# Optimization experiments

Hardware: AMD Instinct MI355X
Metric: run time of the kernel (lower is better)

The kernel has to match this reference:

```python
import jax, jax.numpy as jnp
import numpy as np

N = 50000      # nodes
T = 4          # snapshots
F_IN = 128     # in_channels
H_DIM = 128    # hidden_channels
E = 800000     # edges per snapshot
K = 3          # Chebyshev order


def _edge_norm(src, dst, n):
    # PyG ChebConv sym normalization with lambda_max=2.0:
    # L_hat = L - I = -D^{-1/2} A D^{-1/2}  (diagonal of L_hat is 0)
    ones = jnp.ones(src.shape[0], jnp.float32)
    deg = jax.ops.segment_sum(ones, src, num_segments=n)
    dinv = jnp.where(deg > 0, jax.lax.rsqrt(deg), 0.0)
    return -dinv[src] * dinv[dst]


def _cheb_conv(x, src, dst, w, W, b):
    # x:(N,Fi), W:(K,Fi,Fo), b:(Fo,). Tx_0=x, Tx_1=L_hat x, Tx_k=2 L_hat Tx_{k-1} - Tx_{k-2}
    n = x.shape[0]

    def prop(t):  # sparse matmul L_hat @ t via gather-scale-scatter
        return jax.ops.segment_sum(w[:, None] * t[src], dst, num_segments=n)

    Tx0 = x
    out = Tx0 @ W[0]
    Tx1 = prop(Tx0)
    out = out + Tx1 @ W[1]
    for k in range(2, K):
        Tx2 = 2.0 * prop(Tx1) - Tx0
        out = out + Tx2 @ W[k]
        Tx0, Tx1 = Tx1, Tx2
    return out + b


def setup_inputs() -> dict:
    key = jax.random.key(0)
    ks = jax.random.split(key, 12)
    x = jax.random.normal(ks[0], (T, N, F_IN), jnp.float32)
    edge_index = jax.random.randint(ks[1], (T, 2, E), 0, N, dtype=jnp.int64)

    def w(k, fi, fo):
        return jax.random.normal(k, (K, fi, fo), jnp.float32) * 0.05

    inp = {
        "x": x, "edge_index": edge_index,
        "Wxz": w(ks[2], F_IN, H_DIM), "Whz": w(ks[3], H_DIM, H_DIM),
        "Wxr": w(ks[4], F_IN, H_DIM), "Whr": w(ks[5], H_DIM, H_DIM),
        "Wxh": w(ks[6], F_IN, H_DIM), "Whh": w(ks[7], H_DIM, H_DIM),
        "bxz": jnp.zeros(H_DIM, jnp.float32), "bhz": jnp.zeros(H_DIM, jnp.float32),
        "bxr": jnp.zeros(H_DIM, jnp.float32), "bhr": jnp.zeros(H_DIM, jnp.float32),
        "bxh": jnp.zeros(H_DIM, jnp.float32), "bhh": jnp.zeros(H_DIM, jnp.float32),
        "Wd1": jax.random.normal(ks[8], (H_DIM, H_DIM), jnp.float32) * 0.05,
        "bd1": jnp.zeros(H_DIM, jnp.float32),
        "Wd2": jax.random.normal(ks[9], (H_DIM, F_IN), jnp.float32) * 0.05,
        "bd2": jnp.zeros(F_IN, jnp.float32),
    }
    return inp


def reference(x, edge_index, Wxz, Whz, Wxr, Whr, Wxh, Whh,
              bxz, bhz, bxr, bhr, bxh, bhh, Wd1, bd1, Wd2, bd2):
    n = x.shape[1]

    def step(H, inp):
        xt, ei = inp
        src, dst = ei[0], ei[1]
        w = _edge_norm(src, dst, n)
        Z = jax.nn.sigmoid(_cheb_conv(xt, src, dst, w, Wxz, bxz)
                           + _cheb_conv(H, src, dst, w, Whz, bhz))
        R = jax.nn.sigmoid(_cheb_conv(xt, src, dst, w, Wxr, bxr)
                           + _cheb_conv(H, src, dst, w, Whr, bhr))
        Ht = jnp.tanh(_cheb_conv(xt, src, dst, w, Wxh, bxh)
                      + _cheb_conv(H * R, src, dst, w, Whh, bhh))
        H = Z * H + (1.0 - Z) * Ht
        return H, None

    H0 = jnp.zeros((n, H_DIM), x.dtype)
    H, _ = jax.lax.scan(step, H0, (x, edge_index))
    # decoder (dropout is identity at inference)
    x_pred = jax.nn.relu(H @ Wd1 + bd1) @ Wd2 + bd2
    return x_pred, H
```

## Files before the change

kernel.cpp:

```cpp
#include <hip/hip_runtime.h>
#include <math.h>

#define NN 50000
#define TT 4
#define FF 128
#define EE 800000
#define NSEG 4
#define BINSEG 12500
#define NCH 32
#define CHUNK 25000
#define NCH2 128
#define CH2 6250
#define NB2 64
#define CB 782
#define NSEG2 16
#define SEGW 3125
#define SBINS (CB*NSEG2)
#define SCHUNK 49
#define SMAX 13312
#define SPB 2048

typedef __attribute__((ext_vector_type(8))) short bf8_t;
typedef __attribute__((ext_vector_type(4))) float f4_t;
typedef __attribute__((ext_vector_type(8))) ushort us8;

__device__ inline ushort f2bf(float f){
  union { float f; unsigned u; } v; v.f = f;
  unsigned u = v.u;
  unsigned r = (u + 0x7fff + ((u>>16)&1)) >> 16;
  return (ushort)r;
}
__device__ inline float lo16(unsigned u){ union{unsigned u;float f;}v; v.u=u<<16; return v.f; }
__device__ inline float hi16(unsigned u){ union{unsigned u;float f;}v; v.u=u&0xffff0000u; return v.f; }
__device__ inline unsigned packbf(float x, float y){
  return (unsigned)f2bf(x) | ((unsigned)f2bf(y)<<16);
}
__device__ inline float sigm(float x){ return 1.f/(1.f+expf(-x)); }


__global__ void k_cast4(const float* __restrict__ in, ushort* __restrict__ outp, int n4){
  int i = blockIdx.x*256 + threadIdx.x;
  if(i<n4){
    float4 v = ((const float4*)in)[i];
    ushort4 o; o.x=f2bf(v.x); o.y=f2bf(v.y); o.z=f2bf(v.z); o.w=f2bf(v.w);
    int t = i / (NN*32);
    int rem = i - t*(NN*32);
    int r = rem >> 5;
    int f = (rem & 31) * 4;
    *(ushort4*)(outp + (size_t)t*NN*128 + ((size_t)(f>>5)*NN + r)*32 + (f&31)) = o;
  }
}
__global__ void k_bias(const float* bxz, const float* bhz, const float* bxr,
                       const float* bhr, const float* bxh, const float* bhh,
                       float* __restrict__ bz, float* __restrict__ br, float* __restrict__ bh){
  int i = threadIdx.x;
  int c = i & 127, s = i >> 7;
  if(s==0) bz[c]=bxz[c]+bhz[c];
  else if(s==1) br[c]=bxr[c]+bhr[c];
  else bh[c]=bxh[c]+bhh[c];
}

__global__ __launch_bounds__(256) void k_hist(const int* __restrict__ ei,
                                              int* __restrict__ part){
  int c = blockIdx.x, seg = blockIdx.y, t = blockIdx.z;
  const int* keys = ei + (size_t)t*2*EE;
  __shared__ int h[BINSEG];
  for(int i=threadIdx.x;i<BINSEG;i+=256) h[i]=0;
  __syncthreads();
  int base = seg*BINSEG;
  int e0 = c*CHUNK, e1 = e0+CHUNK;
  for(int e=e0+threadIdx.x; e<e1; e+=256){
    int k = keys[e] - base;
    if((unsigned)k < (unsigned)BINSEG) atomicAdd(&h[k],1);
  }
  __syncthreads();
  int* dp = part + ((((size_t)t)*NSEG + seg)*NCH + c)*BINSEG;
  for(int i=threadIdx.x;i<BINSEG;i+=256) dp[i]=h[i];
}
__global__ void k_merge(const int* __restrict__ part, float* __restrict__ dinv4){
  int t = blockIdx.y;
  int n = blockIdx.x*256 + threadIdx.x;
  if(n>=NN) return;
  int seg = n / BINSEG, b = n - seg*BINSEG;
  const int* p = part + ((((size_t)t)*NSEG + seg)*NCH)*BINSEG + b;
  int s = 0;
  #pragma unroll
  for(int c=0;c<NCH;++c) s += p[(size_t)c*BINSEG];
  dinv4[(size_t)t*NN + n] = s>0 ? rsqrtf((float)s) : 0.f;
}

__global__ __launch_bounds__(256) void k_ccount(const int* __restrict__ ei,
                                                int* __restrict__ ccnt){
  int c = blockIdx.x, t = blockIdx.y;
  const int* dst = ei + (size_t)t*2*EE + EE;
  __shared__ int h[NB2];
  if(threadIdx.x<NB2) h[threadIdx.x]=0;
  __syncthreads();
  int e0 = c*CH2, e1 = e0+CH2;
  for(int e=e0+threadIdx.x; e<e1; e+=256) atomicAdd(&h[dst[e]/CB],1);
  __syncthreads();
  if(threadIdx.x<NB2) ccnt[((size_t)t*NB2 + threadIdx.x)*NCH2 + c] = h[threadIdx.x];
}
__global__ __launch_bounds__(128) void k_cscan(const int* __restrict__ ccnt,
                        int* __restrict__ Abase, int* __restrict__ Bbase,
                        int* __restrict__ tot){
  int t = blockIdx.x, tid = threadIdx.x;
  __shared__ int st[NB2];
  __shared__ int sb[NB2];
  const int* cc = ccnt + (size_t)t*NB2*NCH2;
  if(tid<NB2){
    int s=0;
    for(int c=0;c<NCH2;++c) s += cc[tid*NCH2+c];
    st[tid]=s;
  }
  __syncthreads();
  if(tid==0){
    int run=0;
    for(int b=0;b<NB2;++b){ sb[b]=run; run+=st[b]; }
  }
  __syncthreads();
  if(tid<NB2){
    Bbase[t*NB2+tid]=sb[tid];
    tot[t*NB2+tid]=st[tid];
    int run = sb[tid];
    int* ab = Abase + ((size_t)t*NB2 + tid)*NCH2;
    for(int c=0;c<NCH2;++c){ ab[c]=run; run+=cc[tid*NCH2+c]; }
  }
}
__global__ __launch_bounds__(256) void k_part(const int* __restrict__ ei,
                        const int* __restrict__ Abase, unsigned* __restrict__ staging){
  int c = blockIdx.x, t = blockIdx.y;
  const int* src = ei + (size_t)t*2*EE;
  const int* dst = src + EE;
  unsigned* stg = staging + (size_t)t*EE;
  const int* ab = Abase + (size_t)t*NB2*NCH2;
  __shared__ int h[NB2];
  if(threadIdx.x<NB2) h[threadIdx.x]=0;
  __syncthreads();
  int e0 = c*CH2, e1 = e0+CH2;
  for(int e=e0+threadIdx.x; e<e1; e+=256){
    int s=src[e], d=dst[e];
    int b = d/CB, dl = d - b*CB;
    int r = atomicAdd(&h[b],1);
    stg[ab[b*NCH2 + c] + r] = ((unsigned)dl<<16) | (unsigned)s;
  }
}
__global__ __launch_bounds__(256) void k_sortb(const unsigned* __restrict__ staging,
                        const int* __restrict__ Bbase, const int* __restrict__ tot,
                        const float* __restrict__ dinv4, int2* __restrict__ meta4,
                        int* __restrict__ offs4){
  int b = blockIdx.x, t = blockIdx.y, tid = threadIdx.x;
  __shared__ int cnt[SBINS];
  __shared__ int sums[256];
  __shared__ unsigned sorted[SMAX];
  int sA = Bbase[t*NB2+b];
  int nb = tot[t*NB2+b];
  const unsigned* stg = staging + (size_t)t*EE + sA;
  const float* dinv = dinv4 + (size_t)t*NN;
  int* offs = offs4 + (size_t)t*(NN+1);
  int2* meta = meta4 + (size_t)t*EE + sA;
  for(int i=tid;i<SBINS;i+=256) cnt[i]=0;
  __syncthreads();
  for(int i=tid;i<nb;i+=256){
    unsigned v = stg[i];
    int key = (int)(v>>16)*NSEG2 + (int)(v&0xFFFF)/SEGW;
    atomicAdd(&cnt[key],1);
  }
  __syncthreads();
  int base = tid*SCHUNK;
  int s0 = 0;
  for(int j=0;j<SCHUNK;++j){ int idx=base+j; if(idx<SBINS) s0+=cnt[idx]; }
  sums[tid]=s0; __syncthreads();
  for(int off=1;off<256;off<<=1){
    int v=(tid>=off)?sums[tid-off]:0; __syncthreads();
    sums[tid]+=v; __syncthreads();
  }
  int run = sums[tid]-s0;
  for(int j=0;j<SCHUNK;++j){
    int idx=base+j;
    if(idx<SBINS){ int c=cnt[idx]; cnt[idx]=run; run+=c; }
  }
  __syncthreads();
  for(int dl=tid; dl<CB; dl+=256){
    int n = b*CB + dl;
    if(n<=NN) offs[n] = sA + cnt[dl*NSEG2];
  }
  __syncthreads();
  for(int i=tid;i<nb;i+=256){
    unsigned v = stg[i];
    int key = (int)(v>>16)*NSEG2 + (int)(v&0xFFFF)/SEGW;
    int r = atomicAdd(&cnt[key],1);
    if(r<SMAX) sorted[r]=v;
  }
  __syncthreads();
  for(int i=tid;i<nb;i+=256){
    if(i>=SMAX) break;
    unsigned v = sorted[i];
    int s = v & 0xFFFF, d = b*CB + (v>>16);
    int2 m; m.x = s; m.y = __float_as_int(-dinv[s]*dinv[d]);
    meta[i]=m;
  }
}

__global__ __launch_bounds__(256) void k_spmm2q(const int* __restrict__ offs,
                        const int2* __restrict__ meta,
                        const ushort* __restrict__ Xa, const ushort* __restrict__ Xb,
                        ushort* __restrict__ outA, ushort* __restrict__ outB){
  int bid = blockIdx.x;
  int q = (bid & 7) >> 1;
  int rank = ((bid >> 3) << 1) | (bid & 1);
  int g = threadIdx.x >> 4, l = threadIdx.x & 15;
  const unsigned* XA = (const unsigned*)Xa + (size_t)q*NN*16;
  const unsigned* XB = (const unsigned*)Xb + (size_t)q*NN*16;
  unsigned* OA = (unsigned*)outA + (size_t)q*NN*16;
  unsigned* OB = (unsigned*)outB + (size_t)q*NN*16;
  for(int row = rank*16 + g; row < NN; row += (SPB/4)*16){
    int beg = offs[row], end = offs[row+1];
    float ax=0.f, ay=0.f, bx=0.f, by=0.f;
    int e = beg;
    for(; e+3<end; e+=4){
      int2 p0=meta[e+0], p1=meta[e+1], p2=meta[e+2], p3=meta[e+3];
      float w0=__int_as_float(p0.y), w1=__int_as_float(p1.y);
      float w2=__int_as_float(p2.y), w3=__int_as_float(p3.y);
      unsigned a0=XA[(size_t)p0.x*16+l], a1=XA[(size_t)p1.x*16+l];
      unsigned a2=XA[(size_t)p2.x*16+l], a3=XA[(size_t)p3.x*16+l];
      unsigned b0=XB[(size_t)p0.x*16+l], b1=XB[(size_t)p1.x*16+l];
      unsigned b2=XB[(size_t)p2.x*16+l], b3=XB[(size_t)p3.x*16+l];
      ax=fmaf(w0,lo16(a0),ax); ay=fmaf(w0,hi16(a0),ay);
      ax=fmaf(w1,lo16(a1),ax); ay=fmaf(w1,hi16(a1),ay);
      ax=fmaf(w2,lo16(a2),ax); ay=fmaf(w2,hi16(a2),ay);
      ax=fmaf(w3,lo16(a3),ax); ay=fmaf(w3,hi16(a3),ay);
      bx=fmaf(w0,lo16(b0),bx); by=fmaf(w0,hi16(b0),by);
      bx=fmaf(w1,lo16(b1),bx); by=fmaf(w1,hi16(b1),by);
      bx=fmaf(w2,lo16(b2),bx); by=fmaf(w2,hi16(b2),by);
      bx=fmaf(w3,lo16(b3),bx); by=fmaf(w3,hi16(b3),by);
    }
    for(; e<end; ++e){
      int2 pm=meta[e]; float w=__int_as_float(pm.y);
      unsigned a=XA[(size_t)pm.x*16+l], b=XB[(size_t)pm.x*16+l];
      ax=fmaf(w,lo16(a),ax); ay=fmaf(w,hi16(a),ay);
      bx=fmaf(w,lo16(b),bx); by=fmaf(w,hi16(b),by);
    }
    OA[(size_t)row*16 + l] = packbf(ax, ay);
    OB[(size_t)row*16 + l] = packbf(bx, by);
  }
}
__global__ __launch_bounds__(256) void k_spmm1q(const int* __restrict__ offs,
                        const int2* __restrict__ meta,
                        const ushort* __restrict__ Xa, ushort* __restrict__ outA){
  int bid = blockIdx.x;
  int q = (bid & 7) >> 1;
  int rank = ((bid >> 3) << 1) | (bid & 1);
  int g = threadIdx.x >> 4, l = threadIdx.x & 15;
  const unsigned* XA = (const unsigned*)Xa + (size_t)q*NN*16;
  unsigned* OA = (unsigned*)outA + (size_t)q*NN*16;
  for(int row = rank*16 + g; row < NN; row += (SPB/4)*16){
    int beg = offs[row], end = offs[row+1];
    float ax=0.f, ay=0.f;
    int e = beg;
    for(; e+3<end; e+=4){
      int2 p0=meta[e+0], p1=meta[e+1], p2=meta[e+2], p3=meta[e+3];
      float w0=__int_as_float(p0.y), w1=__int_as_float(p1.y);
      float w2=__int_as_float(p2.y), w3=__int_as_float(p3.y);
      unsigned a0=XA[(size_t)p0.x*16+l], a1=XA[(size_t)p1.x*16+l];
      unsigned a2=XA[(size_t)p2.x*16+l], a3=XA[(size_t)p3.x*16+l];
      ax=fmaf(w0,lo16(a0),ax); ay=fmaf(w0,hi16(a0),ay);
      ax=fmaf(w1,lo16(a1),ax); ay=fmaf(w1,hi16(a1),ay);
      ax=fmaf(w2,lo16(a2),ax); ay=fmaf(w2,hi16(a2),ay);
      ax=fmaf(w3,lo16(a3),ax); ay=fmaf(w3,hi16(a3),ay);
    }
    for(; e<end; ++e){
      int2 pm=meta[e]; float w=__int_as_float(pm.y);
      unsigned a=XA[(size_t)pm.x*16+l];
      ax=fmaf(w,lo16(a),ax); ay=fmaf(w,hi16(a),ay);
    }
    OA[(size_t)row*16 + l] = packbf(ax, ay);
  }
}

__global__ __launch_bounds__(256) void k_mgemm(
    const ushort* __restrict__ A0, const ushort* __restrict__ A1,
    const ushort* __restrict__ A2, const ushort* __restrict__ A3,
    const ushort* __restrict__ A4, const ushort* __restrict__ A5,
    const ushort* __restrict__ Bt, ushort* __restrict__ Cb, float* __restrict__ Cf,
    int K, int ldb, int ngrp, int bnstep, int coloff, int mode, int nwg,
    const float* __restrict__ bias)
{
  __shared__ ushort As[128*64];
  __shared__ ushort Bs[128*64];
  int tid = threadIdx.x;
  int lane = tid & 63;
  int wid = tid >> 6;
  int wr = (wid>>1)*64, wc = (wid&1)*64;
  int bid = blockIdx.x;
  int q = nwg >> 3, r = nwg & 7;
  int xs = bid & 7, j = bid >> 3;
  int logical = xs*q + ((xs<r)?xs:r) + j;
  int bm = logical / ngrp;
  int bn = (logical - bm*ngrp) * bnstep;
  f4_t acc[4][4] = {};
  int srow = tid>>3, sc = tid&7;
  int lr = lane&15, lk = lane>>4;
  int nkt = K>>6;
  for(int kt=0; kt<nkt; ++kt){
    int k0 = kt<<6;
    const ushort* Ac = (k0<128)?A0:(k0<256)?A1:(k0<384)?A2:(k0<512)?A3:(k0<640)?A4:A5;
    int kloc = k0 & 127;
    int f0 = kloc + sc*8;
    size_t aoff = ((size_t)(f0>>5)*NN)*32 + (f0&31);
    #pragma unroll
    for(int p=0;p<4;++p){
      int rr = srow + p*32;
      int gr = bm*128 + rr; if(gr>=NN) gr=NN-1;
      us8 av = *(const us8*)(Ac + aoff + (size_t)gr*32);
      us8 bv = *(const us8*)(Bt + (size_t)(bn*128 + rr)*ldb + k0 + sc*8);
      int wo = (rr*128 + ((sc*16) ^ ((rr&7)<<4))) >> 1;
      *(us8*)(As + wo) = av;
      *(us8*)(Bs + wo) = bv;
    }
    __syncthreads();
    #pragma unroll
    for(int kk=0;kk<2;++kk){
      bf8_t af[4], bfr[4];
      int co = kk*64 + lk*16;
      #pragma unroll
      for(int m=0;m<4;++m){
        int Ra = wr + m*16 + lr;
        af[m]  = *(const bf8_t*)(As + ((Ra*128 + (co ^ ((Ra&7)<<4)))>>1));
        int Rb = wc + m*16 + lr;
        bfr[m] = *(const bf8_t*)(Bs + ((Rb*128 + (co ^ ((Rb&7)<<4)))>>1));
      }
      #pragma unroll
      for(int m=0;m<4;++m)
        #pragma unroll
        for(int n=0;n<4;++n)
          acc[m][n] = __builtin_amdgcn_mfma_f32_16x16x32_bf16(af[m], bfr[n], acc[m][n], 0,0,0);
    }
    __syncthreads();
  }
  int row0 = bm*128 + wr + lk*4;
  int col0 = bn*128 + wc + lr;
  #pragma unroll
  for(int m=0;m<4;++m){
    #pragma unroll
    for(int i=0;i<4;++i){
      int rI = row0 + m*16 + i;
      if(rI<NN){
        if(mode<=1){
          float* cp = Cf + (size_t)rI*384 + coloff + col0;
          #pragma unroll
          for(int n=0;n<4;++n){
            float v = acc[m][n][i];
            if(mode==1) v += cp[n*16];
            cp[n*16] = v;
          }
        } else if(mode==2){
          #pragma unroll
          for(int n=0;n<4;++n){
            int c = col0 + n*16;
            float v = acc[m][n][i] + bias[c];
            Cb[((size_t)(c>>5)*NN + rI)*32 + (c&31)] = f2bf(fmaxf(v,0.f));
          }
        } else {
          #pragma unroll
          for(int n=0;n<4;++n){
            int c = col0 + n*16;
            Cf[(size_t)rI*128 + c] = acc[m][n][i] + bias[c];
          }
        }
      }
    }
  }
}

__global__ void k_combA(const float* __restrict__ OX, const float* __restrict__ H,
                        const float* __restrict__ bz, const float* __restrict__ br,
                        float* __restrict__ Z, ushort* __restrict__ HRb){
  int i = blockIdx.x*256 + threadIdx.x;
  if(i>=NN*FF) return;
  int r = i>>7, c = i&127;
  float zv = sigm(OX[r*384+c]     + bz[c]);
  float rv = sigm(OX[r*384+128+c] + br[c]);
  float hr = H[i]*rv;
  Z[i]=zv;
  HRb[((size_t)(c>>5)*NN + r)*32 + (c&31)] = f2bf(hr);
}
__global__ void k_combB(const float* __restrict__ OX, const float* __restrict__ Z,
                        const float* __restrict__ H, const float* __restrict__ bh,
                        float* __restrict__ Hn, ushort* __restrict__ Hnb,
                        float* __restrict__ Hout2){
  int i = blockIdx.x*256 + threadIdx.x;
  if(i>=NN*FF) return;
  int r = i>>7, c = i&127;
  float ht = tanhf(OX[r*384+256+c] + bh[c]);
  float z = Z[i];
  float hn = z*H[i] + (1.f-z)*ht;
  Hn[i] = hn;
  Hnb[((size_t)(c>>5)*NN + r)*32 + (c&31)] = f2bf(hn);
  if(Hout2) Hout2[i] = hn;
}
__global__ void k_gru0(const float* __restrict__ OX, const float* __restrict__ bz,
                       const float* __restrict__ bh, float* __restrict__ Hn,
                       ushort* __restrict__ Hnb){
  int i = blockIdx.x*256 + threadIdx.x;
  if(i>=NN*FF) return;
  int r = i>>7, c = i&127;
  float z  = sigm(OX[r*384+c] + bz[c]);
  float ht = tanhf(OX[r*384+256+c] + bh[c]);
  float hn = (1.f - z)*ht;
  Hn[i]=hn;
  Hnb[((size_t)(c>>5)*NN + r)*32 + (c&31)] = f2bf(hn);
}

__global__ void k_packx(const float* __restrict__ Wxz, const float* __restrict__ Wxr,
                        const float* __restrict__ Wxh, const float* __restrict__ Whz,
                        const float* __restrict__ Whr, ushort* __restrict__ Bt){
  int i = blockIdx.x*256 + threadIdx.x;
  if(i>=384*768) return;
  int c = i/768, k = i - c*768;
  int g = c>>7, j = c&127;
  int kb = k>>7, kk = k&127;
  float v;
  int e = kk*128 + j;
  if(kb<3){
    const float* W = (g==0)?Wxz:((g==1)?Wxr:Wxh);
    v = (kb==0) ? (W[e] - W[2*16384 + e]) : (kb==1 ? W[16384 + e] : 2.f*W[2*16384 + e]);
  } else if(g<2){
    const float* W = (g==0)?Whz:Whr;
    int kb2 = kb-3;
    v = (kb2==0) ? (W[e] - W[2*16384 + e]) : (kb2==1 ? W[16384 + e] : 2.f*W[2*16384 + e]);
  } else v = 0.f;
  Bt[i] = f2bf(v);
}
__global__ void k_packh(const float* __restrict__ Whh, ushort* __restrict__ Bt){
  int i = blockIdx.x*256 + threadIdx.x;
  if(i>=128*384) return;
  int c = i/384, k = i - c*384;
  int kb = k>>7, kk = k&127;
  int e = kk*128 + c;
  float v = (kb==0) ? (Whh[e] - Whh[2*16384 + e]) : (kb==1 ? Whh[16384 + e] : 2.f*Whh[2*16384 + e]);
  Bt[i] = f2bf(v);
}
__global__ void k_packd(const float* __restrict__ W, ushort* __restrict__ Bt){
  int i = blockIdx.x*256 + threadIdx.x;
  if(i>=128*128) return;
  int c = i>>7, k = i&127;
  Bt[i] = f2bf(W[k*128 + c]);
}

extern "C" void kernel_launch(void* const* d_in, const int* in_sizes, int n_in,
                              void* d_out, int out_size, void* d_ws, size_t ws_size,
                              hipStream_t stream) {
  const float* x   = (const float*)d_in[0];
  const int*   ei  = (const int*)d_in[1];
  const float* Wxz = (const float*)d_in[2];
  const float* Whz = (const float*)d_in[3];
  const float* Wxr = (const float*)d_in[4];
  const float* Whr = (const float*)d_in[5];
  const float* Wxh = (const float*)d_in[6];
  const float* Whh = (const float*)d_in[7];
  const float* bxz = (const float*)d_in[8];
  const float* bhz = (const float*)d_in[9];
  const float* bxr = (const float*)d_in[10];
  const float* bhr = (const float*)d_in[11];
  const float* bxh = (const float*)d_in[12];
  const float* bhh = (const float*)d_in[13];
  const float* Wd1 = (const float*)d_in[14];
  const float* bd1 = (const float*)d_in[15];
  const float* Wd2 = (const float*)d_in[16];
  const float* bd2 = (const float*)d_in[17];
  float* out = (float*)d_out;

  char* p = (char*)d_ws;
  auto alloc = [&](size_t bytes)->void*{ void* r = (void*)p; p += (bytes+255)&~(size_t)255; return r; };
  const size_t NFB  = (size_t)NN*FF*4;
  const size_t NFB2 = (size_t)NN*FF*2;
  float* Ha   = (float*)alloc(NFB);
  float* Hb   = (float*)alloc(NFB);
  float* OX   = (float*)alloc((size_t)NN*384*4);
  float* Zb   = (float*)alloc(NFB);
  ushort* xtb4= (ushort*)alloc(NFB2*TT);
  ushort* A1b = (ushort*)alloc(NFB2);
  ushort* A2b = (ushort*)alloc(NFB2);
  ushort* A3b = (ushort*)alloc(NFB2);
  ushort* A4b = (ushort*)alloc(NFB2);
  ushort* HRb = (ushort*)alloc(NFB2);
  ushort* Hab = (ushort*)alloc(NFB2);
  ushort* Hbb = (ushort*)alloc(NFB2);
  ushort* Btx = (ushort*)alloc((size_t)384*768*2);
  ushort* Bth = (ushort*)alloc((size_t)128*384*2);
  ushort* Btd1= (ushort*)alloc((size_t)128*128*2);
  ushort* Btd2= (ushort*)alloc((size_t)128*128*2);
  float* bzc  = (float*)alloc(128*4);
  float* brc  = (float*)alloc(128*4);
  float* bhc  = (float*)alloc(128*4);
  float* dinv4= (float*)alloc((size_t)TT*NN*4);
  int* ccnt   = (int*)alloc((size_t)TT*NB2*NCH2*4);
  int* Abase  = (int*)alloc((size_t)TT*NB2*NCH2*4);
  int* Bbase  = (int*)alloc((size_t)TT*NB2*4);
  int* tot    = (int*)alloc((size_t)TT*NB2*4);
  int* offs4  = (int*)alloc((size_t)TT*(NN+1)*4);
  int2* meta4 = (int2*)alloc((size_t)TT*EE*8);
  int* partial = (int*)Ha;
  unsigned* staging = (unsigned*)Hb;

  const int fb = (NN*FF+255)/256;
  const int MT = (NN+127)/128;

  k_packx<<<(384*768+255)/256,256,0,stream>>>(Wxz,Wxr,Wxh,Whz,Whr,Btx);
  k_packh<<<(128*384+255)/256,256,0,stream>>>(Whh,Bth);
  k_packd<<<64,256,0,stream>>>(Wd1,Btd1);
  k_packd<<<64,256,0,stream>>>(Wd2,Btd2);
  k_bias<<<1,384,0,stream>>>(bxz,bhz,bxr,bhr,bxh,bhh,bzc,brc,bhc);
  k_cast4<<<(TT*NN*FF/4+255)/256,256,0,stream>>>(x, xtb4, TT*NN*FF/4);
  dim3 gh(NCH, NSEG, TT);
  k_hist<<<gh,256,0,stream>>>(ei, partial);
  dim3 gm((NN+255)/256, TT);
  k_merge<<<gm,256,0,stream>>>(partial, dinv4);
  dim3 gc(NCH2, TT);
  k_ccount<<<gc,256,0,stream>>>(ei, ccnt);
  k_cscan<<<TT,128,0,stream>>>(ccnt, Abase, Bbase, tot);
  k_part<<<gc,256,0,stream>>>(ei, Abase, staging);
  dim3 gs(NB2, TT);
  k_sortb<<<gs,256,0,stream>>>(staging, Bbase, tot, dinv4, meta4, offs4);

  float* Hc = Ha; float* Hn = Hb;
  ushort* Hcb = Hab; ushort* Hnb = Hbb;
  for(int t=0;t<TT;++t){
    const ushort* xtb = xtb4 + (size_t)t*NN*FF;
    const int* offs = offs4 + (size_t)t*(NN+1);
    const int2* meta = meta4 + (size_t)t*EE;
    if(t==0){
      k_spmm1q<<<SPB,256,0,stream>>>(offs,meta, xtb, A1b);
      k_spmm1q<<<SPB,256,0,stream>>>(offs,meta, A1b, A2b);
      int nwg0 = MT*2;
      k_mgemm<<<nwg0,256,0,stream>>>(xtb,A1b,A2b,nullptr,nullptr,nullptr,
          Btx, nullptr, OX, 384, 768, 2, 2, 0, 0, nwg0, nullptr);
      k_gru0<<<fb,256,0,stream>>>(OX, bzc, bhc, Hn, Hnb);
    } else {
      k_spmm2q<<<SPB,256,0,stream>>>(offs,meta, xtb,Hcb, A1b,A3b);
      k_spmm2q<<<SPB,256,0,stream>>>(offs,meta, A1b,A3b, A2b,A4b);
      int nwg1 = MT*3;
      k_mgemm<<<nwg1,256,0,stream>>>(xtb,A1b,A2b,Hcb,A3b,A4b,
          Btx, nullptr, OX, 768, 768, 3, 1, 0, 0, nwg1, nullptr);
      k_combA<<<fb,256,0,stream>>>(OX,Hc,bzc,brc,Zb,HRb);
      k_spmm1q<<<SPB,256,0,stream>>>(offs,meta, HRb, A3b);
      k_spmm1q<<<SPB,256,0,stream>>>(offs,meta, A3b, A4b);
      int nwg3 = MT;
      k_mgemm<<<nwg3,256,0,stream>>>(HRb,A3b,A4b,nullptr,nullptr,nullptr,
          Bth, nullptr, OX, 384, 384, 1, 1, 256, 1, nwg3, nullptr);
      float* hout2 = (t==TT-1) ? (out + (size_t)NN*FF) : nullptr;
      k_combB<<<fb,256,0,stream>>>(OX,Zb,Hc,bhc,Hn,Hnb,hout2);
    }
    float* tmp=Hc; Hc=Hn; Hn=tmp;
    ushort* tb=Hcb; Hcb=Hnb; Hnb=tb;
  }
  k_mgemm<<<MT,256,0,stream>>>(Hcb,nullptr,nullptr,nullptr,nullptr,nullptr,
      Btd1, A1b, nullptr, 128, 128, 1, 1, 0, 2, MT, bd1);
  k_mgemm<<<MT,256,0,stream>>>(A1b,nullptr,nullptr,nullptr,nullptr,nullptr,
      Btd2, nullptr, out, 128, 128, 1, 1, 0, 3, MT, bd2);
}
```

Before: 1.355 ms.

## Split SpMM rows across a full wave and drop dual-input SpMM kernel

```diff
diff --git a/kernel.cpp b/kernel.cpp
--- a/kernel.cpp
+++ b/kernel.cpp
@@ -202,79 +202,33 @@
   }
 }
 
-__global__ __launch_bounds__(256) void k_spmm2q(const int* __restrict__ offs,
-                        const int2* __restrict__ meta,
-                        const ushort* __restrict__ Xa, const ushort* __restrict__ Xb,
-                        ushort* __restrict__ outA, ushort* __restrict__ outB){
-  int bid = blockIdx.x;
-  int q = (bid & 7) >> 1;
-  int rank = ((bid >> 3) << 1) | (bid & 1);
-  int g = threadIdx.x >> 4, l = threadIdx.x & 15;
-  const unsigned* XA = (const unsigned*)Xa + (size_t)q*NN*16;
-  const unsigned* XB = (const unsigned*)Xb + (size_t)q*NN*16;
-  unsigned* OA = (unsigned*)outA + (size_t)q*NN*16;
-  unsigned* OB = (unsigned*)outB + (size_t)q*NN*16;
-  for(int row = rank*16 + g; row < NN; row += (SPB/4)*16){
-    int beg = offs[row], end = offs[row+1];
-    float ax=0.f, ay=0.f, bx=0.f, by=0.f;
-    int e = beg;
-    for(; e+3<end; e+=4){
-      int2 p0=meta[e+0], p1=meta[e+1], p2=meta[e+2], p3=meta[e+3];
-      float w0=__int_as_float(p0.y), w1=__int_as_float(p1.y);
-      float w2=__int_as_float(p2.y), w3=__int_as_float(p3.y);
-      unsigned a0=XA[(size_t)p0.x*16+l], a1=XA[(size_t)p1.x*16+l];
-      unsigned a2=XA[(size_t)p2.x*16+l], a3=XA[(size_t)p3.x*16+l];
-      unsigned b0=XB[(size_t)p0.x*16+l], b1=XB[(size_t)p1.x*16+l];
-      unsigned b2=XB[(size_t)p2.x*16+l], b3=XB[(size_t)p3.x*16+l];
-      ax=fmaf(w0,lo16(a0),ax); ay=fmaf(w0,hi16(a0),ay);
-      ax=fmaf(w1,lo16(a1),ax); ay=fmaf(w1,hi16(a1),ay);
-      ax=fmaf(w2,lo16(a2),ax); ay=fmaf(w2,hi16(a2),ay);
-      ax=fmaf(w3,lo16(a3),ax); ay=fmaf(w3,hi16(a3),ay);
-      bx=fmaf(w0,lo16(b0),bx); by=fmaf(w0,hi16(b0),by);
-      bx=fmaf(w1,lo16(b1),bx); by=fmaf(w1,hi16(b1),by);
-      bx=fmaf(w2,lo16(b2),bx); by=fmaf(w2,hi16(b2),by);
-      bx=fmaf(w3,lo16(b3),bx); by=fmaf(w3,hi16(b3),by);
-    }
-    for(; e<end; ++e){
-      int2 pm=meta[e]; float w=__int_as_float(pm.y);
-      unsigned a=XA[(size_t)pm.x*16+l], b=XB[(size_t)pm.x*16+l];
-      ax=fmaf(w,lo16(a),ax); ay=fmaf(w,hi16(a),ay);
-      bx=fmaf(w,lo16(b),bx); by=fmaf(w,hi16(b),by);
-    }
-    OA[(size_t)row*16 + l] = packbf(ax, ay);
-    OB[(size_t)row*16 + l] = packbf(bx, by);
-  }
-}
 __global__ __launch_bounds__(256) void k_spmm1q(const int* __restrict__ offs,
                         const int2* __restrict__ meta,
                         const ushort* __restrict__ Xa, ushort* __restrict__ outA){
   int bid = blockIdx.x;
   int q = (bid & 7) >> 1;
   int rank = ((bid >> 3) << 1) | (bid & 1);
-  int g = threadIdx.x >> 4, l = threadIdx.x & 15;
+  int wid = threadIdx.x >> 6;
+  int waveIdx = rank*4 + wid;
+  int g = (threadIdx.x >> 4) & 3;
+  int l = threadIdx.x & 15;
   const unsigned* XA = (const unsigned*)Xa + (size_t)q*NN*16;
   unsigned* OA = (unsigned*)outA + (size_t)q*NN*16;
-  for(int row = rank*16 + g; row < NN; row += (SPB/4)*16){
+  const long long* mp = (const long long*)meta;
+  for(int row = waveIdx; row < NN; row += SPB){
     int beg = offs[row], end = offs[row+1];
     float ax=0.f, ay=0.f;
-    int e = beg;
-    for(; e+3<end; e+=4){
-      int2 p0=meta[e+0], p1=meta[e+1], p2=meta[e+2], p3=meta[e+3];
-      float w0=__int_as_float(p0.y), w1=__int_as_float(p1.y);
-      float w2=__int_as_float(p2.y), w3=__int_as_float(p3.y);
-      unsigned a0=XA[(size_t)p0.x*16+l], a1=XA[(size_t)p1.x*16+l];
-      unsigned a2=XA[(size_t)p2.x*16+l], a3=XA[(size_t)p3.x*16+l];
-      ax=fmaf(w0,lo16(a0),ax); ay=fmaf(w0,hi16(a0),ay);
-      ax=fmaf(w1,lo16(a1),ax); ay=fmaf(w1,hi16(a1),ay);
-      ax=fmaf(w2,lo16(a2),ax); ay=fmaf(w2,hi16(a2),ay);
-      ax=fmaf(w3,lo16(a3),ax); ay=fmaf(w3,hi16(a3),ay);
+    for(int e = beg + g; e < end; e += 4){
+      long long mv = __builtin_nontemporal_load(mp + e);
+      int s = (int)(unsigned)(mv & 0xffffffffLL);
+      float w = __int_as_float((int)(mv >> 32));
+      unsigned a = XA[(size_t)s*16 + l];
+      ax = fmaf(w, lo16(a), ax);
+      ay = fmaf(w, hi16(a), ay);
     }
-    for(; e<end; ++e){
-      int2 pm=meta[e]; float w=__int_as_float(pm.y);
-      unsigned a=XA[(size_t)pm.x*16+l];
-      ax=fmaf(w,lo16(a),ax); ay=fmaf(w,hi16(a),ay);
-    }
-    OA[(size_t)row*16 + l] = packbf(ax, ay);
+    ax += __shfl_xor(ax, 16); ax += __shfl_xor(ax, 32);
+    ay += __shfl_xor(ay, 16); ay += __shfl_xor(ay, 32);
+    if(g==0) __builtin_nontemporal_store(packbf(ax, ay), OA + (size_t)row*16 + l);
   }
 }
 
@@ -538,8 +492,10 @@
           Btx, nullptr, OX, 384, 768, 2, 2, 0, 0, nwg0, nullptr);
       k_gru0<<<fb,256,0,stream>>>(OX, bzc, bhc, Hn, Hnb);
     } else {
-      k_spmm2q<<<SPB,256,0,stream>>>(offs,meta, xtb,Hcb, A1b,A3b);
-      k_spmm2q<<<SPB,256,0,stream>>>(offs,meta, A1b,A3b, A2b,A4b);
+      k_spmm1q<<<SPB,256,0,stream>>>(offs,meta, xtb, A1b);
+      k_spmm1q<<<SPB,256,0,stream>>>(offs,meta, Hcb, A3b);
+      k_spmm1q<<<SPB,256,0,stream>>>(offs,meta, A1b, A2b);
+      k_spmm1q<<<SPB,256,0,stream>>>(offs,meta, A3b, A4b);
       int nwg1 = MT*3;
       k_mgemm<<<nwg1,256,0,stream>>>(xtb,A1b,A2b,Hcb,A3b,A4b,
           Btx, nullptr, OX, 768, 768, 3, 1, 0, 0, nwg1, nullptr);
```

Result: slower. 2.784 ms (+105.4%).
